# Performance work log

Measured on AMD Instinct MI355X. Metric: run time of the kernel, lower is better.

Reference implementation:

```python
import jax, jax.numpy as jnp
import numpy as np

H = 64  # hidden_size

def _lstm_layer(x_tbd, W_ih, W_hh, b_ih, b_hh):
    """x_tbd: [T, B, D] -> outputs [T, B, H]. PyTorch gate order i,f,g,o."""
    T, B, _ = x_tbd.shape
    # input contribution precomputed for all timesteps: [T, B, 4H]
    xg = jnp.einsum('tbd,gd->tbg', x_tbd, W_ih) + b_ih + b_hh

    def step(carry, xg_t):
        h, c = carry
        gates = xg_t + h @ W_hh.T  # [B, 4H]
        i, f, g, o = jnp.split(gates, 4, axis=-1)
        i = jax.nn.sigmoid(i)
        f = jax.nn.sigmoid(f)
        g = jnp.tanh(g)
        o = jax.nn.sigmoid(o)
        c = f * c + i * g
        h = o * jnp.tanh(c)
        return (h, c), h

    h0 = jnp.zeros((B, H), dtype=x_tbd.dtype)
    c0 = jnp.zeros((B, H), dtype=x_tbd.dtype)
    _, hs = jax.lax.scan(step, (h0, c0), xg)
    return hs  # [T, B, H]


def setup_inputs() -> dict:
    key = jax.random.key(0)
    ks = jax.random.split(key, 16)
    B, T, D = 1024, 512, 32
    s = 1.0 / np.sqrt(H)  # PyTorch LSTM init scale
    return {
        'x': jax.random.normal(ks[0], (B, T, D), dtype=jnp.float32),
        'W_ih_l0': jax.random.uniform(ks[1], (4 * H, D), jnp.float32, -s, s),
        'W_hh_l0': jax.random.uniform(ks[2], (4 * H, H), jnp.float32, -s, s),
        'b_ih_l0': jax.random.uniform(ks[3], (4 * H,), jnp.float32, -s, s),
        'b_hh_l0': jax.random.uniform(ks[4], (4 * H,), jnp.float32, -s, s),
        'W_ih_l1': jax.random.uniform(ks[5], (4 * H, H), jnp.float32, -s, s),
        'W_hh_l1': jax.random.uniform(ks[6], (4 * H, H), jnp.float32, -s, s),
        'b_ih_l1': jax.random.uniform(ks[7], (4 * H,), jnp.float32, -s, s),
        'b_hh_l1': jax.random.uniform(ks[8], (4 * H,), jnp.float32, -s, s),
        'fc1_w': jax.random.uniform(ks[9], (H // 2, H), jnp.float32, -s, s),
        'fc1_b': jax.random.uniform(ks[10], (H // 2,), jnp.float32, -s, s),
        'fc2_w': jax.random.uniform(ks[11], (1, H // 2), jnp.float32, -0.25, 0.25),
        'fc2_b': jax.random.uniform(ks[12], (1,), jnp.float32, -0.25, 0.25),
    }


def reference(x, W_ih_l0, W_hh_l0, b_ih_l0, b_hh_l0,
              W_ih_l1, W_hh_l1, b_ih_l1, b_hh_l1,
              fc1_w, fc1_b, fc2_w, fc2_b):
    x_tbd = jnp.transpose(x, (1, 0, 2))  # [T, B, D]
    h1 = _lstm_layer(x_tbd, W_ih_l0, W_hh_l0, b_ih_l0, b_hh_l0)   # [T, B, H]
    h2 = _lstm_layer(h1,   W_ih_l1, W_hh_l1, b_ih_l1, b_hh_l1)   # [T, B, H]
    last = h2[-1]                       # [B, H] == lstm_out[:, -1, :]
    out = jax.nn.relu(last @ fc1_w.T + fc1_b)  # dropout is identity at eval
    out = out @ fc2_w.T + fc2_b         # [B, 1]
    return out
```

## Files before the change

kernel.cpp:

```cpp
#include <hip/hip_runtime.h>
#include <math.h>
#include <stdint.h>


namespace {

constexpr int Hh = 64, Dd = 32, Tt = 512;
constexpr float LOG2E = 1.4426950408889634f;

typedef _Float16 f16x8 __attribute__((ext_vector_type(8)));
typedef float f32x4 __attribute__((ext_vector_type(4)));

__device__ __forceinline__ f32x4 mfma(f16x8 a, f16x8 b, f32x4 c) {
    return __builtin_amdgcn_mfma_f32_16x16x32_f16(a, b, c, 0, 0, 0);
}
__device__ __forceinline__ float rcpf(float x) { return __builtin_amdgcn_rcpf(x); }
__device__ __forceinline__ float exp2f_(float x) { return __builtin_amdgcn_exp2f(x); }
__device__ __forceinline__ float sigm_s(float p) { return rcpf(1.0f + exp2f_(-p)); }
__device__ __forceinline__ float tanh_s(float p) {
    return 1.0f - 2.0f * rcpf(exp2f_(p) + 1.0f);
}
__device__ __forceinline__ float tanh_n(float c) {
    return 1.0f - 2.0f * rcpf(exp2f_(c * (2.0f * LOG2E)) + 1.0f);
}
__device__ __forceinline__ f16x8 cvt8s(const float* p, float sc) {
    f16x8 r;
#pragma unroll
    for (int e = 0; e < 8; ++e) r[e] = (_Float16)(p[e] * sc);
    return r;
}
__device__ __forceinline__ uint32_t pack2(_Float16 a, _Float16 b) {
    union { _Float16 h[2]; uint32_t u; } p;
    p.h[0] = a; p.h[1] = b;
    return p.u;
}
__device__ __forceinline__ void bar_lgkm() {
    asm volatile("s_waitcnt lgkmcnt(0)\n\ts_barrier" ::: "memory");
}

__global__ __launch_bounds__(512, 2) void lstm_f16(
    const float* __restrict__ x,
    const float* __restrict__ Wih0,
    const float* __restrict__ Whh0,
    const float* __restrict__ bih0, const float* __restrict__ bhh0,
    const float* __restrict__ Wih1,
    const float* __restrict__ Whh1,
    const float* __restrict__ bih1, const float* __restrict__ bhh1,
    const float* __restrict__ fc1w,
    const float* __restrict__ fc1b,
    const float* __restrict__ fc2w,
    const float* __restrict__ fc2b,
    float* __restrict__ out)
{
    __shared__ __align__(16) _Float16 s_x[2][64][8];
    __shared__ __align__(16) _Float16 s_h0[2][2][64][8];
    __shared__ __align__(16) _Float16 s_h1[2][2][64][8];
    __shared__ float s_hf[Hh][9];
    __shared__ float s_fcw[32 * 65];
    __shared__ float s_fc[32][9];

    const int tid = threadIdx.x;
    const int w = tid >> 6;
    const int l = tid & 63;
    const int ar = l & 15;
    const int akb = l >> 4;
    const int cq = l >> 4;
    const int cj = l & 15;
    const int b0 = blockIdx.x * 8;
    const bool isL1 = (cj >= 8);
    const int cb = cj & 7;

    const int r4 = ar & 3;
    const float sc = (r4 == 2) ? 2.0f * LOG2E : LOG2E;
    const int gbase = r4 * 64 + 8 * w + 2 * (ar >> 2);
    f16x8 A0x[2], A0h[2][2], A1a[2][2], A1b[2][2];
#pragma unroll
    for (int i = 0; i < 2; ++i) {
        const int g = gbase + i;
        A0x[i] = cvt8s(Wih0 + g * Dd + akb * 8, sc);
#pragma unroll
        for (int kt = 0; kt < 2; ++kt) {
            A0h[i][kt] = cvt8s(Whh0 + g * Hh + kt * 32 + akb * 8, sc);
            A1a[i][kt] = cvt8s(Wih1 + g * Hh + kt * 32 + akb * 8, sc);
            A1b[i][kt] = cvt8s(Whh1 + g * Hh + kt * 32 + akb * 8, sc);
        }
    }
    const int ub = 8 * w + 2 * cq;
    f32x4 bias0[2], bias1[2];
#pragma unroll
    for (int i = 0; i < 2; ++i)
#pragma unroll
        for (int r = 0; r < 4; ++r) {
            const float s2 = (r == 2) ? 2.0f * LOG2E : LOG2E;
            bias0[i][r] = s2 * (bih0[r * 64 + ub + i] + bhh0[r * 64 + ub + i]);
            bias1[i][r] = s2 * (bih1[r * 64 + ub + i] + bhh1[r * 64 + ub + i]);
        }

    const int kt_h = w >> 2;
    const int fl_h = (w & 3) * 16 + cb;
    _Float16* const wbase = isL1 ? &s_h1[1][kt_h][fl_h][2 * cq]
                                 : &s_h0[0][kt_h][fl_h][2 * cq];
    const int wdelta = isL1 ? -1024 : 1024;

    const int kx = tid & 31;
    const int bx = (tid >> 5) & 7;
    const int flx = ((kx >> 3) << 4) | bx;
    const int ex = kx & 7;
    const float* xp = x + ((size_t)(b0 + bx) * Tt) * Dd + kx;

    ((int*)s_h0)[tid] = 0; ((int*)s_h0)[tid + 512] = 0;
    ((int*)s_h1)[tid] = 0; ((int*)s_h1)[tid + 512] = 0;

    float rx0 = 0.f, rx1 = 0.f;
    if (tid < 256) {
        const _Float16 v0 = (_Float16)xp[0];
        s_x[0][flx][ex] = v0;
        s_x[0][flx + 8][ex] = v0;
        rx0 = xp[Dd];
        rx1 = xp[2 * Dd];
    }
    float cst[2] = {0.f, 0.f};
    __syncthreads();

    for (int t = 0; t < Tt; ++t) {
        const int pr = t & 1;
        if (tid < 256) {
            const _Float16 v = (_Float16)rx0;
            s_x[pr ^ 1][flx][ex] = v;
            s_x[pr ^ 1][flx + 8][ex] = v;
            rx0 = rx1;
            const int tn = (t + 3 < Tt) ? (t + 3) : (Tt - 1);
            rx1 = xp[(size_t)tn * Dd];
        }
        const f16x8 bxv = *(const f16x8*)&s_x[pr][l][0];
        const f16x8 b0a = *(const f16x8*)&s_h0[pr ^ 1][0][l][0];
        const f16x8 b0b = *(const f16x8*)&s_h0[pr ^ 1][1][l][0];
        const f16x8 b1a = *(const f16x8*)&s_h1[pr][0][l][0];
        const f16x8 b1b = *(const f16x8*)&s_h1[pr][1][l][0];

        f32x4 gg[2];
#pragma unroll
        for (int i = 0; i < 2; ++i) {
            f32x4 a = bias0[i];
            a = mfma(A0x[i], bxv, a);
            a = mfma(A0h[i][0], b0a, a);
            a = mfma(A0h[i][1], b0b, a);
            f32x4 b = bias1[i];
            b = mfma(A1a[i][0], b0a, b);
            b = mfma(A1a[i][1], b0b, b);
            b = mfma(A1b[i][0], b1a, b);
            b = mfma(A1b[i][1], b1b, b);
#pragma unroll
            for (int r = 0; r < 4; ++r) gg[i][r] = isL1 ? b[r] : a[r];
        }

        _Float16 hp[2];
#pragma unroll
        for (int i = 0; i < 2; ++i) {
            const float gi = sigm_s(gg[i][0]);
            const float gf = sigm_s(gg[i][1]);
            const float zz = tanh_s(gg[i][2]);
            const float go = sigm_s(gg[i][3]);
            float cn = gf * cst[i] + gi * zz;
            float hv = go * tanh_n(cn);
            if (t == 0) {
                cn = isL1 ? 0.f : cn;
                hv = isL1 ? 0.f : hv;
            }
            cst[i] = cn;
            hp[i] = (_Float16)hv;
        }
        const uint32_t packed = pack2(hp[0], hp[1]);
        _Float16* wp = wbase + (pr ? wdelta : 0);
        *(uint32_t*)wp = packed;
        *(uint32_t*)(wp + 64) = packed;
        bar_lgkm();
    }

    {
        const f16x8 b0a = *(const f16x8*)&s_h0[1][0][l][0];
        const f16x8 b0b = *(const f16x8*)&s_h0[1][1][l][0];
        const f16x8 b1a = *(const f16x8*)&s_h1[0][0][l][0];
        const f16x8 b1b = *(const f16x8*)&s_h1[0][1][l][0];
#pragma unroll
        for (int i = 0; i < 2; ++i) {
            f32x4 b = bias1[i];
            b = mfma(A1a[i][0], b0a, b);
            b = mfma(A1a[i][1], b0b, b);
            b = mfma(A1b[i][0], b1a, b);
            b = mfma(A1b[i][1], b1b, b);
            if (isL1) {
                const float gi = sigm_s(b[0]);
                const float gf = sigm_s(b[1]);
                const float zz = tanh_s(b[2]);
                const float go = sigm_s(b[3]);
                const float cn = gf * cst[i] + gi * zz;
                s_hf[ub + i][cb] = go * tanh_n(cn);
            }
        }
    }
    __syncthreads();

    for (int i2 = tid; i2 < 32 * 64; i2 += 512) {
        const int m = i2 >> 6, uu = i2 & 63;
        s_fcw[m * 65 + uu] = fc1w[i2];
    }
    __syncthreads();
    if (tid < 256) {
        const int m = tid >> 3, jj = tid & 7;
        float acc = fc1b[m];
#pragma unroll
        for (int uu = 0; uu < Hh; ++uu)
            acc = fmaf(s_fcw[m * 65 + uu], s_hf[uu][jj], acc);
        s_fc[m][jj] = fmaxf(acc, 0.f);
    }
    __syncthreads();
    if (tid < 8) {
        float acc = fc2b[0];
#pragma unroll
        for (int m = 0; m < 32; ++m)
            acc = fmaf(fc2w[m], s_fc[m][tid], acc);
        out[b0 + tid] = acc;
    }
}

}

extern "C" void kernel_launch(void* const* d_in, const int* in_sizes, int n_in,
                              void* d_out, int out_size, void* d_ws, size_t ws_size,
                              hipStream_t stream) {
    const float* x    = (const float*)d_in[0];
    const float* Wih0 = (const float*)d_in[1];
    const float* Whh0 = (const float*)d_in[2];
    const float* bih0 = (const float*)d_in[3];
    const float* bhh0 = (const float*)d_in[4];
    const float* Wih1 = (const float*)d_in[5];
    const float* Whh1 = (const float*)d_in[6];
    const float* bih1 = (const float*)d_in[7];
    const float* bhh1 = (const float*)d_in[8];
    const float* fc1w = (const float*)d_in[9];
    const float* fc1b = (const float*)d_in[10];
    const float* fc2w = (const float*)d_in[11];
    const float* fc2b = (const float*)d_in[12];
    float* out = (float*)d_out;

    lstm_f16<<<dim3(128), dim3(512), 0, stream>>>(
        x, Wih0, Whh0, bih0, bhh0, Wih1, Whh1, bih1, bhh1,
        fc1w, fc1b, fc2w, fc2b, out);
}
```

Before: 327.0 us.

## Split batch into 4-row blocks of 4 waves, each wave covering more gate rows

```diff
diff --git a/kernel.cpp b/kernel.cpp
--- a/kernel.cpp
+++ b/kernel.cpp
@@ -38,7 +38,7 @@
     asm volatile("s_waitcnt lgkmcnt(0)\n\ts_barrier" ::: "memory");
 }
 
-__global__ __launch_bounds__(512, 2) void lstm_f16(
+__global__ __launch_bounds__(256, 1) void lstm_f16(
     const float* __restrict__ x,
     const float* __restrict__ Wih0,
     const float* __restrict__ Whh0,
@@ -52,12 +52,11 @@
     const float* __restrict__ fc2b,
     float* __restrict__ out)
 {
-    __shared__ __align__(16) _Float16 s_x[2][64][8];
     __shared__ __align__(16) _Float16 s_h0[2][2][64][8];
     __shared__ __align__(16) _Float16 s_h1[2][2][64][8];
-    __shared__ float s_hf[Hh][9];
+    __shared__ float s_hf[Hh][5];
     __shared__ float s_fcw[32 * 65];
-    __shared__ float s_fc[32][9];
+    __shared__ float s_fc[32][5];
 
     const int tid = threadIdx.x;
     const int w = tid >> 6;
@@ -66,17 +65,18 @@
     const int akb = l >> 4;
     const int cq = l >> 4;
     const int cj = l & 15;
-    const int b0 = blockIdx.x * 8;
-    const bool isL1 = (cj >= 8);
-    const int cb = cj & 7;
+    const int cb = cj & 3;
+    const int dsel = (cj >> 2) & 1;
+    const bool isL1 = (cj & 8) != 0;
+    const int b0 = blockIdx.x * 4;
 
     const int r4 = ar & 3;
     const float sc = (r4 == 2) ? 2.0f * LOG2E : LOG2E;
-    const int gbase = r4 * 64 + 8 * w + 2 * (ar >> 2);
-    f16x8 A0x[2], A0h[2][2], A1a[2][2], A1b[2][2];
-#pragma unroll
-    for (int i = 0; i < 2; ++i) {
-        const int g = gbase + i;
+    const int grow = r4 * 64 + 16 * w + 4 * (ar >> 2);
+    f16x8 A0x[4], A0h[4][2], A1a[4][2], A1b[4][2];
+#pragma unroll
+    for (int i = 0; i < 4; ++i) {
+        const int g = grow + i;
         A0x[i] = cvt8s(Wih0 + g * Dd + akb * 8, sc);
 #pragma unroll
         for (int kt = 0; kt < 2; ++kt) {
@@ -85,95 +85,109 @@
             A1b[i][kt] = cvt8s(Whh1 + g * Hh + kt * 32 + akb * 8, sc);
         }
     }
-    const int ub = 8 * w + 2 * cq;
-    f32x4 bias0[2], bias1[2];
-#pragma unroll
-    for (int i = 0; i < 2; ++i)
+
+    const int ub = 16 * w + 4 * cq + 2 * dsel;
+    const float* bi = isL1 ? bih1 : bih0;
+    const float* bh = isL1 ? bhh1 : bhh0;
+    f32x4 biasSel[2];
+#pragma unroll
+    for (int j = 0; j < 2; ++j)
 #pragma unroll
         for (int r = 0; r < 4; ++r) {
             const float s2 = (r == 2) ? 2.0f * LOG2E : LOG2E;
-            bias0[i][r] = s2 * (bih0[r * 64 + ub + i] + bhh0[r * 64 + ub + i]);
-            bias1[i][r] = s2 * (bih1[r * 64 + ub + i] + bhh1[r * 64 + ub + i]);
-        }
-
-    const int kt_h = w >> 2;
-    const int fl_h = (w & 3) * 16 + cb;
-    _Float16* const wbase = isL1 ? &s_h1[1][kt_h][fl_h][2 * cq]
-                                 : &s_h0[0][kt_h][fl_h][2 * cq];
+            biasSel[j][r] = s2 * (bi[r * 64 + ub + j] + bh[r * 64 + ub + j]);
+        }
+
+    const int kt_h = ub >> 5;
+    const int q_h = (ub & 31) >> 3;
+    const int e_h = ub & 7;
+    _Float16* const wsel = isL1 ? &s_h1[1][kt_h][q_h * 16 + cb][e_h]
+                                : &s_h0[0][kt_h][q_h * 16 + cb][e_h];
     const int wdelta = isL1 ? -1024 : 1024;
 
-    const int kx = tid & 31;
-    const int bx = (tid >> 5) & 7;
-    const int flx = ((kx >> 3) << 4) | bx;
-    const int ex = kx & 7;
-    const float* xp = x + ((size_t)(b0 + bx) * Tt) * Dd + kx;
-
-    ((int*)s_h0)[tid] = 0; ((int*)s_h0)[tid + 512] = 0;
-    ((int*)s_h1)[tid] = 0; ((int*)s_h1)[tid + 512] = 0;
-
-    float rx0 = 0.f, rx1 = 0.f;
-    if (tid < 256) {
-        const _Float16 v0 = (_Float16)xp[0];
-        s_x[0][flx][ex] = v0;
-        s_x[0][flx + 8][ex] = v0;
-        rx0 = xp[Dd];
-        rx1 = xp[2 * Dd];
-    }
+    const float* xbase = x + ((size_t)(b0 + cb) * Tt) * Dd + akb * 8;
+
+#pragma unroll
+    for (int k = 0; k < 4; ++k) {
+        ((int*)s_h0)[tid + 256 * k] = 0;
+        ((int*)s_h1)[tid + 256 * k] = 0;
+    }
+
+    float4 xr0 = *(const float4*)(xbase);
+    float4 xr1 = *(const float4*)(xbase + 4);
+    f16x8 xcur;
+#pragma unroll
+    for (int e = 0; e < 4; ++e) {
+        xcur[e] = (_Float16)xr0[e];
+        xcur[4 + e] = (_Float16)xr1[e];
+    }
+    xr0 = *(const float4*)(xbase + Dd);
+    xr1 = *(const float4*)(xbase + Dd + 4);
+
     float cst[2] = {0.f, 0.f};
     __syncthreads();
 
+#pragma unroll 2
     for (int t = 0; t < Tt; ++t) {
         const int pr = t & 1;
-        if (tid < 256) {
-            const _Float16 v = (_Float16)rx0;
-            s_x[pr ^ 1][flx][ex] = v;
-            s_x[pr ^ 1][flx + 8][ex] = v;
-            rx0 = rx1;
-            const int tn = (t + 3 < Tt) ? (t + 3) : (Tt - 1);
-            rx1 = xp[(size_t)tn * Dd];
-        }
-        const f16x8 bxv = *(const f16x8*)&s_x[pr][l][0];
         const f16x8 b0a = *(const f16x8*)&s_h0[pr ^ 1][0][l][0];
         const f16x8 b0b = *(const f16x8*)&s_h0[pr ^ 1][1][l][0];
         const f16x8 b1a = *(const f16x8*)&s_h1[pr][0][l][0];
         const f16x8 b1b = *(const f16x8*)&s_h1[pr][1][l][0];
 
-        f32x4 gg[2];
-#pragma unroll
-        for (int i = 0; i < 2; ++i) {
-            f32x4 a = bias0[i];
-            a = mfma(A0x[i], bxv, a);
+        f32x4 gA[4], gB[4];
+#pragma unroll
+        for (int i = 0; i < 4; ++i) {
+            f32x4 a = {0.f, 0.f, 0.f, 0.f};
+            a = mfma(A0x[i], xcur, a);
             a = mfma(A0h[i][0], b0a, a);
             a = mfma(A0h[i][1], b0b, a);
-            f32x4 b = bias1[i];
+            gA[i] = a;
+            f32x4 b = {0.f, 0.f, 0.f, 0.f};
             b = mfma(A1a[i][0], b0a, b);
             b = mfma(A1a[i][1], b0b, b);
             b = mfma(A1b[i][0], b1a, b);
             b = mfma(A1b[i][1], b1b, b);
-#pragma unroll
-            for (int r = 0; r < 4; ++r) gg[i][r] = isL1 ? b[r] : a[r];
-        }
+            gB[i] = b;
+        }
+
+        f16x8 xn;
+#pragma unroll
+        for (int e = 0; e < 4; ++e) {
+            xn[e] = (_Float16)xr0[e];
+            xn[4 + e] = (_Float16)xr1[e];
+        }
+        const int tf = (t + 2 < Tt) ? (t + 2) : (Tt - 1);
+        xr0 = *(const float4*)(xbase + (size_t)tf * Dd);
+        xr1 = *(const float4*)(xbase + (size_t)tf * Dd + 4);
+        xcur = xn;
 
         _Float16 hp[2];
 #pragma unroll
-        for (int i = 0; i < 2; ++i) {
-            const float gi = sigm_s(gg[i][0]);
-            const float gf = sigm_s(gg[i][1]);
-            const float zz = tanh_s(gg[i][2]);
-            const float go = sigm_s(gg[i][3]);
-            float cn = gf * cst[i] + gi * zz;
+        for (int j = 0; j < 2; ++j) {
+            const f32x4 sA = dsel ? gA[2 + j] : gA[j];
+            const f32x4 sB = dsel ? gB[2 + j] : gB[j];
+            f32x4 gg = isL1 ? sB : sA;
+            gg += biasSel[j];
+            const float gi = sigm_s(gg[0]);
+            const float gf = sigm_s(gg[1]);
+            const float zz = tanh_s(gg[2]);
+            const float go = sigm_s(gg[3]);
+            float cn = gf * cst[j] + gi * zz;
             float hv = go * tanh_n(cn);
             if (t == 0) {
                 cn = isL1 ? 0.f : cn;
                 hv = isL1 ? 0.f : hv;
             }
-            cst[i] = cn;
-            hp[i] = (_Float16)hv;
-        }
-        const uint32_t packed = pack2(hp[0], hp[1]);
-        _Float16* wp = wbase + (pr ? wdelta : 0);
-        *(uint32_t*)wp = packed;
-        *(uint32_t*)(wp + 64) = packed;
+            cst[j] = cn;
+            hp[j] = (_Float16)hv;
+        }
+        const uint32_t pk = pack2(hp[0], hp[1]);
+        _Float16* wp = wsel + (pr ? wdelta : 0);
+        *(uint32_t*)(wp) = pk;
+        *(uint32_t*)(wp + 32) = pk;
+        *(uint32_t*)(wp + 64) = pk;
+        *(uint32_t*)(wp + 96) = pk;
         bar_lgkm();
     }
 
@@ -182,32 +196,39 @@
         const f16x8 b0b = *(const f16x8*)&s_h0[1][1][l][0];
         const f16x8 b1a = *(const f16x8*)&s_h1[0][0][l][0];
         const f16x8 b1b = *(const f16x8*)&s_h1[0][1][l][0];
-#pragma unroll
-        for (int i = 0; i < 2; ++i) {
-            f32x4 b = bias1[i];
+        f32x4 gB[4];
+#pragma unroll
+        for (int i = 0; i < 4; ++i) {
+            f32x4 b = {0.f, 0.f, 0.f, 0.f};
             b = mfma(A1a[i][0], b0a, b);
             b = mfma(A1a[i][1], b0b, b);
             b = mfma(A1b[i][0], b1a, b);
             b = mfma(A1b[i][1], b1b, b);
-            if (isL1) {
-                const float gi = sigm_s(b[0]);
-                const float gf = sigm_s(b[1]);
-                const float zz = tanh_s(b[2]);
-                const float go = sigm_s(b[3]);
-                const float cn = gf * cst[i] + gi * zz;
-                s_hf[ub + i][cb] = go * tanh_n(cn);
+            gB[i] = b;
+        }
+        if (isL1) {
+#pragma unroll
+            for (int j = 0; j < 2; ++j) {
+                f32x4 gg = dsel ? gB[2 + j] : gB[j];
+                gg += biasSel[j];
+                const float gi = sigm_s(gg[0]);
+                const float gf = sigm_s(gg[1]);
+                const float zz = tanh_s(gg[2]);
+                const float go = sigm_s(gg[3]);
+                const float cn = gf * cst[j] + gi * zz;
+                s_hf[ub + j][cb] = go * tanh_n(cn);
             }
         }
     }
     __syncthreads();
 
-    for (int i2 = tid; i2 < 32 * 64; i2 += 512) {
+    for (int i2 = tid; i2 < 32 * 64; i2 += 256) {
         const int m = i2 >> 6, uu = i2 & 63;
         s_fcw[m * 65 + uu] = fc1w[i2];
     }
     __syncthreads();
-    if (tid < 256) {
-        const int m = tid >> 3, jj = tid & 7;
+    if (tid < 128) {
+        const int m = tid >> 2, jj = tid & 3;
         float acc = fc1b[m];
 #pragma unroll
         for (int uu = 0; uu < Hh; ++uu)
@@ -215,7 +236,7 @@
         s_fc[m][jj] = fmaxf(acc, 0.f);
     }
     __syncthreads();
-    if (tid < 8) {
+    if (tid < 4) {
         float acc = fc2b[0];
 #pragma unroll
         for (int m = 0; m < 32; ++m)
@@ -244,7 +265,7 @@
     const float* fc2b = (const float*)d_in[12];
     float* out = (float*)d_out;
 
-    lstm_f16<<<dim3(128), dim3(512), 0, stream>>>(
+    lstm_f16<<<dim3(256), dim3(256), 0, stream>>>(
         x, Wih0, Whh0, bih0, bhh0, Wih1, Whh1, bih1, bhh1,
         fc1w, fc1b, fc2w, fc2b, out);
 }
```

Result: slower. 964.2 us (+194.8%).
